# Kernel optimization log

Measured on AMD Instinct MI355X. Metric: run time of the kernel, lower is better.

## Reference

```python
import jax, jax.numpy as jnp
import numpy as np

N_NODES = 50000
N_EDGES = 800000
BATCH = 4


def setup_inputs() -> dict:
    key = jax.random.key(0)
    ks = jax.random.split(key, 12)
    inp = {
        "x": jax.random.normal(ks[0], (BATCH, N_NODES, 1, 1), dtype=jnp.float32),
        "edge_index": jax.random.randint(ks[1], (2, N_EDGES), 0, N_NODES, dtype=jnp.int64),
        "W_conv1": jax.random.normal(ks[2], (3, 1, 32), dtype=jnp.float32) * 0.1,
        "b_conv1": jnp.zeros((3, 32), dtype=jnp.float32),
        "W_lin1": jax.random.normal(ks[3], (3, 64, 32), dtype=jnp.float32) * 0.1,
        "b_lin1": jnp.zeros((3, 32), dtype=jnp.float32),
        "att1": jax.random.uniform(ks[4], (1,), dtype=jnp.float32),
        "W_conv2": jax.random.normal(ks[5], (3, 32, 32), dtype=jnp.float32) * 0.1,
        "b_conv2": jnp.zeros((3, 32), dtype=jnp.float32),
        "W_lin2": jax.random.normal(ks[6], (3, 64, 32), dtype=jnp.float32) * 0.1,
        "b_lin2": jnp.zeros((3, 32), dtype=jnp.float32),
        "att2": jax.random.uniform(ks[7], (1,), dtype=jnp.float32),
        "W_out": jax.random.normal(ks[8], (32, 1), dtype=jnp.float32) * 0.1,
        "b_out": jnp.zeros((1,), dtype=jnp.float32),
    }
    return inp


def _gcn(h, W, b, src, dst, norm, inv_deg, n):
    # h: (B,N,Fin) -> (B,N,Fout); symmetric-normalized GCNConv with self loops
    xw = h @ W                                   # (B,N,Fout)
    msg = xw[:, src, :] * norm[None, :, None]    # (B,E,Fout)
    agg = jax.ops.segment_sum(jnp.swapaxes(msg, 0, 1), dst, num_segments=n)
    agg = jnp.swapaxes(agg, 0, 1)                # (B,N,Fout)
    return agg + xw * inv_deg[None, :, None] + b


def _tgcn_cell(h_in, Wc, bc, Wl, bl, att, src, dst, norm, inv_deg, n):
    # TGCN2 GRU cell with H0 = 0, weighted by softmax(att) (periods=1 -> weight 1)
    B = h_in.shape[0]
    out_dim = Wc.shape[-1]
    H = jnp.zeros((B, n, out_dim), dtype=h_in.dtype)
    cz = _gcn(h_in, Wc[0], bc[0], src, dst, norm, inv_deg, n)
    Z = jax.nn.sigmoid(jnp.concatenate([cz, H], axis=-1) @ Wl[0] + bl[0])
    cr = _gcn(h_in, Wc[1], bc[1], src, dst, norm, inv_deg, n)
    R = jax.nn.sigmoid(jnp.concatenate([cr, H], axis=-1) @ Wl[1] + bl[1])
    ch = _gcn(h_in, Wc[2], bc[2], src, dst, norm, inv_deg, n)
    Ht = jnp.tanh(jnp.concatenate([ch, H * R], axis=-1) @ Wl[2] + bl[2])
    Hn = Z * H + (1.0 - Z) * Ht
    a = jax.nn.softmax(att)  # (1,) -> [1.0]
    return a[0] * Hn


def reference(x, edge_index, W_conv1, b_conv1, W_lin1, b_lin1, att1,
              W_conv2, b_conv2, W_lin2, b_lin2, att2, W_out, b_out):
    n = x.shape[1]
    src, dst = edge_index[0], edge_index[1]
    ones = jnp.ones(src.shape[0], dtype=x.dtype)
    deg = jax.ops.segment_sum(ones, dst, num_segments=n) + 1.0  # + self loop
    dis = jax.lax.rsqrt(deg)
    norm = dis[src] * dis[dst]   # (E,)
    inv_deg = 1.0 / deg          # self-loop norm

    h = x[..., 0]  # (B,N,1) periods=1
    h = jax.nn.relu(_tgcn_cell(h, W_conv1, b_conv1, W_lin1, b_lin1, att1,
                               src, dst, norm, inv_deg, n))
    h = jax.nn.relu(_tgcn_cell(h, W_conv2, b_conv2, W_lin2, b_lin2, att2,
                               src, dst, norm, inv_deg, n))
    return h @ W_out + b_out  # (B,N,1)
```

## Files before the change

### kernel.cpp

```cpp
#include <hip/hip_runtime.h>
#include <hip/hip_fp16.h>
#include <stdint.h>

#define N_NODES 50000
#define BATCH 4
#define CAP 64

__global__ void zero_precomp_kernel(int* __restrict__ cursor,
                                    const float* __restrict__ Wc1,
                                    const float* __restrict__ bc1,
                                    const float* __restrict__ Wl1,
                                    const float* __restrict__ bl1,
                                    const float* __restrict__ Wc2,
                                    const float* __restrict__ bc2,
                                    const float* __restrict__ Wl2,
                                    const float* __restrict__ bl2,
                                    float* __restrict__ pc, int N) {
    int i = blockIdx.x * blockDim.x + threadIdx.x;
    if (i < N) cursor[i] = 0;
    if (i >= 2240) return;
    if (i < 2048) {
        int g = i >> 10;
        int kf = i & 1023;
        int k = kf >> 5, f = kf & 31;
        int gate = g ? 2 : 0;
        float s = 0.0f;
        for (int j = 0; j < 32; ++j)
            s += Wc2[gate * 1024 + k * 32 + j] * Wl2[gate * 2048 + j * 32 + f];
        pc[i] = s;
    } else if (i < 2112) {
        int g = (i - 2048) >> 5;
        int f = i & 31;
        int gate = g ? 2 : 0;
        float s = bl2[gate * 32 + f];
        for (int j = 0; j < 32; ++j)
            s += bc2[gate * 32 + j] * Wl2[gate * 2048 + j * 32 + f];
        pc[i] = s;
    } else {
        int t = i - 2112;
        int which = t >> 5;
        int f = t & 31;
        int gate = (which >= 2) ? 2 : 0;
        if ((which & 1) == 0) {
            float s = 0.0f;
            for (int j = 0; j < 32; ++j)
                s += Wc1[gate * 32 + j] * Wl1[gate * 2048 + j * 32 + f];
            pc[i] = s;
        } else {
            float s = bl1[gate * 32 + f];
            for (int j = 0; j < 32; ++j)
                s += bc1[gate * 32 + j] * Wl1[gate * 2048 + j * 32 + f];
            pc[i] = s;
        }
    }
}

__global__ void fill_kernel(const int* __restrict__ src,
                            const int* __restrict__ dst,
                            int* __restrict__ cursor,
                            unsigned short* __restrict__ bucket, int E) {
    int e = blockIdx.x * blockDim.x + threadIdx.x;
    if (e < E) {
        int d = dst[e];
        int pos = atomicAdd(&cursor[d], 1);
        if (pos < CAP) bucket[d * CAP + pos] = (unsigned short)src[e];
    }
}

__global__ void dis_xd_kernel(const int* __restrict__ deg,
                              const float* __restrict__ x,
                              float* __restrict__ dis,
                              float4* __restrict__ xd, int N) {
    int n = blockIdx.x * blockDim.x + threadIdx.x;
    if (n >= N) return;
    float d = rsqrtf((float)(deg[n] + 1));
    dis[n] = d;
    xd[n] = make_float4(x[n] * d, x[N + n] * d, x[2 * N + n] * d,
                        x[3 * N + n] * d);
}

__global__ void s1h1_kernel(const float4* __restrict__ xd,
                            const float* __restrict__ dis,
                            const int* __restrict__ deg,
                            const unsigned short* __restrict__ bucket,
                            const float* __restrict__ pc,
                            char* __restrict__ hs, int N) {
    int idx = blockIdx.x * blockDim.x + threadIdx.x;
    int node = idx >> 3;
    if (node >= N) return;
    int j = idx & 7;
    int cnt = deg[node];
    if (cnt > CAP) cnt = CAP;
    float ax, ay, az, aw;
    if (j == 0) {
        float4 v = xd[node];
        ax = v.x; ay = v.y; az = v.z; aw = v.w;
    } else {
        ax = ay = az = aw = 0.f;
    }
    for (int i = j; i < cnt; i += 8) {
        int s = bucket[node * CAP + i];
        float4 v = xd[s];
        ax += v.x; ay += v.y; az += v.z; aw += v.w;
    }
#pragma unroll
    for (int m = 4; m; m >>= 1) {
        ax += __shfl_xor(ax, m, 64);
        ay += __shfl_xor(ay, m, 64);
        az += __shfl_xor(az, m, 64);
        aw += __shfl_xor(aw, m, 64);
    }
    float d = dis[node];
    float t0 = ax * d, t1 = ay * d, t2 = az * d, t3 = aw * d;
#pragma unroll
    for (int m = 0; m < 4; ++m) {
        int f = j + 8 * m;
        float uz = pc[2112 + f], vz = pc[2144 + f];
        float uh = pc[2176 + f], vh = pc[2208 + f];
        float h0 = fmaxf((1.0f - 1.0f / (1.0f + expf(-(t0 * uz + vz)))) *
                         tanhf(t0 * uh + vh), 0.0f) * d;
        float h1 = fmaxf((1.0f - 1.0f / (1.0f + expf(-(t1 * uz + vz)))) *
                         tanhf(t1 * uh + vh), 0.0f) * d;
        float h2 = fmaxf((1.0f - 1.0f / (1.0f + expf(-(t2 * uz + vz)))) *
                         tanhf(t2 * uh + vh), 0.0f) * d;
        float h3 = fmaxf((1.0f - 1.0f / (1.0f + expf(-(t3 * uz + vz)))) *
                         tanhf(t3 * uh + vh), 0.0f) * d;
        __half2 lo = __floats2half2_rn(h0, h1);
        __half2 hi = __floats2half2_rn(h2, h3);
        uint2 u;
        u.x = *reinterpret_cast<unsigned int*>(&lo);
        u.y = *reinterpret_cast<unsigned int*>(&hi);
        *reinterpret_cast<uint2*>(hs + (size_t)node * 256 + f * 8) = u;
    }
}

__global__ __launch_bounds__(256) void l2_agg_kernel(
    const char* __restrict__ hs, const float* __restrict__ dis,
    const int* __restrict__ deg, const unsigned short* __restrict__ bucket,
    const float* __restrict__ pc, const float* __restrict__ Wout,
    const float* __restrict__ bout, float* __restrict__ out, int N) {
    __shared__ float2 sT[4][64];
    int wv = threadIdx.x >> 6;
    int lane = threadIdx.x & 63;
    int f = lane & 31;
    int h = lane >> 5;

    float wl0[32], wl2[32];
#pragma unroll
    for (int k = 0; k < 32; ++k) {
        wl0[k] = pc[k * 32 + f];
        wl2[k] = pc[1024 + k * 32 + f];
    }
    float w0 = pc[2048 + f], w2 = pc[2080 + f];
    float wf = Wout[f];
    float bo = bout[0];
    const char* hp = hs + f * 8 + h * 4;

    int wid = (blockIdx.x * blockDim.x + threadIdx.x) >> 6;
    int nw = (gridDim.x * blockDim.x) >> 6;

    for (int node = wid; node < N; node += nw) {
        int cnt = deg[node];
        if (cnt > CAP) cnt = CAP;
        unsigned int bidx = bucket[node * CAP + lane];
        __half2 acc = *(const __half2*)(hp + (size_t)node * 256);
        int i = 0;
        for (; i + 8 <= cnt; i += 8) {
            unsigned int o0 = __builtin_amdgcn_readlane(bidx, i) * 256u;
            unsigned int o1 = __builtin_amdgcn_readlane(bidx, i + 1) * 256u;
            unsigned int o2 = __builtin_amdgcn_readlane(bidx, i + 2) * 256u;
            unsigned int o3 = __builtin_amdgcn_readlane(bidx, i + 3) * 256u;
            unsigned int o4 = __builtin_amdgcn_readlane(bidx, i + 4) * 256u;
            unsigned int o5 = __builtin_amdgcn_readlane(bidx, i + 5) * 256u;
            unsigned int o6 = __builtin_amdgcn_readlane(bidx, i + 6) * 256u;
            unsigned int o7 = __builtin_amdgcn_readlane(bidx, i + 7) * 256u;
            __half2 v0 = *(const __half2*)(hp + o0);
            __half2 v1 = *(const __half2*)(hp + o1);
            __half2 v2 = *(const __half2*)(hp + o2);
            __half2 v3 = *(const __half2*)(hp + o3);
            __half2 v4 = *(const __half2*)(hp + o4);
            __half2 v5 = *(const __half2*)(hp + o5);
            __half2 v6 = *(const __half2*)(hp + o6);
            __half2 v7 = *(const __half2*)(hp + o7);
            __half2 s01 = __hadd2(v0, v1);
            __half2 s23 = __hadd2(v2, v3);
            __half2 s45 = __hadd2(v4, v5);
            __half2 s67 = __hadd2(v6, v7);
            acc = __hadd2(acc, __hadd2(__hadd2(s01, s23), __hadd2(s45, s67)));
        }
        for (; i < cnt; ++i) {
            unsigned int o = __builtin_amdgcn_readlane(bidx, i) * 256u;
            acc = __hadd2(acc, *(const __half2*)(hp + o));
        }
        float2 fa = __half22float2(acc);

        sT[wv][lane] = fa;

        float sz0 = 0.f, sz1 = 0.f, sh0 = 0.f, sh1 = 0.f;
        const float2* tp = &sT[wv][h * 32];
#pragma unroll
        for (int k = 0; k < 32; k += 2) {
            float4 t2 = *(const float4*)&tp[k];
            sz0 += t2.x * wl0[k];     sz1 += t2.y * wl0[k];
            sh0 += t2.x * wl2[k];     sh1 += t2.y * wl2[k];
            sz0 += t2.z * wl0[k + 1]; sz1 += t2.w * wl0[k + 1];
            sh0 += t2.z * wl2[k + 1]; sh1 += t2.w * wl2[k + 1];
        }
        float dn = dis[node];
        float z0 = 1.0f / (1.0f + expf(-(dn * sz0 + w0)));
        float z1 = 1.0f / (1.0f + expf(-(dn * sz1 + w0)));
        float t0 = tanhf(dn * sh0 + w2);
        float t1 = tanhf(dn * sh1 + w2);
        float h20 = fmaxf((1.0f - z0) * t0, 0.0f);
        float h21 = fmaxf((1.0f - z1) * t1, 0.0f);

        float o0 = h20 * wf;
        float o1 = h21 * wf;
#pragma unroll
        for (int d = 16; d; d >>= 1) {
            o0 += __shfl_xor(o0, d, 64);
            o1 += __shfl_xor(o1, d, 64);
        }
        if (f == 0) {
            out[(size_t)(2 * h) * N + node] = o0 + bo;
            out[(size_t)(2 * h + 1) * N + node] = o1 + bo;
        }
    }
}


extern "C" void kernel_launch(void* const* d_in, const int* in_sizes, int n_in,
                              void* d_out, int out_size, void* d_ws,
                              size_t ws_size, hipStream_t stream) {
    const float* x    = (const float*)d_in[0];
    const int*   ei   = (const int*)d_in[1];
    const float* Wc1  = (const float*)d_in[2];
    const float* bc1  = (const float*)d_in[3];
    const float* Wl1  = (const float*)d_in[4];
    const float* bl1  = (const float*)d_in[5];
    const float* Wc2  = (const float*)d_in[7];
    const float* bc2  = (const float*)d_in[8];
    const float* Wl2  = (const float*)d_in[9];
    const float* bl2  = (const float*)d_in[10];
    const float* Wout = (const float*)d_in[12];
    const float* bout = (const float*)d_in[13];

    const int E = in_sizes[1] / 2;
    const int N = N_NODES;
    const int* src = ei;
    const int* dst = ei + E;

    char* p = (char*)d_ws;
    auto alloc = [&](size_t bytes) {
        char* r = p;
        p += (bytes + 15) & ~(size_t)15;
        return r;
    };
    int*            cursor = (int*)alloc(N * sizeof(int));
    unsigned short* bucket = (unsigned short*)alloc((size_t)N * CAP * 2);
    float*          dis    = (float*)alloc(N * sizeof(float));
    float*          xd     = (float*)alloc((size_t)N * 4 * sizeof(float));
    char*           hs     = (char*)alloc((size_t)N * 256);
    float*          pc     = (float*)alloc(2240 * sizeof(float));

    zero_precomp_kernel<<<(N + 255) / 256, 256, 0, stream>>>(
        cursor, Wc1, bc1, Wl1, bl1, Wc2, bc2, Wl2, bl2, pc, N);

    fill_kernel<<<(E + 255) / 256, 256, 0, stream>>>(src, dst, cursor, bucket,
                                                     E);
    dis_xd_kernel<<<(N + 255) / 256, 256, 0, stream>>>(cursor, x, dis,
                                                       (float4*)xd, N);
    s1h1_kernel<<<(N * 8 + 255) / 256, 256, 0, stream>>>(
        (const float4*)xd, dis, cursor, bucket, pc, hs, N);

    l2_agg_kernel<<<2048, 256, 0, stream>>>(hs, dis, cursor, bucket, pc, Wout,
                                            bout, (float*)d_out, N);
}
```

Before: 219.1 us.

## Bin neighbor lists by source chunk and process eight nodes per wave in phase

The bucket fill now splits each node's neighbor list into four sub-buckets keyed by source-node range, with a per-chunk cursor. The layer-2 aggregation has each wave handle eight nodes at once, walking the source chunks in lockstep so concurrent gathers hit a narrower slice of the feature table, which aims to improve L2/cache locality. Costs include larger cursor and bucket arrays, more atomics contention patterns, per-chunk caps of 32 that can drop edges for skewed degree, more register pressure, and a per-edge branch on counts.

New measurement: 315.1 us. 43.8% more time.

```diff
diff --git a/kernel.cpp b/kernel.cpp
--- a/kernel.cpp
+++ b/kernel.cpp
@@ -3,10 +3,14 @@
 #include <stdint.h>
 
 #define N_NODES 50000
-#define BATCH 4
-#define CAP 64
-
-__global__ void zero_precomp_kernel(int* __restrict__ cursor,
+#define NC 4
+#define CHUNK 12500
+#define SCAP 32
+#define ROWS 128
+#define ROWU 64
+#define NPW 8
+
+__global__ void zero_precomp_kernel(int* __restrict__ cursor4,
                                     const float* __restrict__ Wc1,
                                     const float* __restrict__ bc1,
                                     const float* __restrict__ Wl1,
@@ -15,9 +19,9 @@
                                     const float* __restrict__ bc2,
                                     const float* __restrict__ Wl2,
                                     const float* __restrict__ bl2,
-                                    float* __restrict__ pc, int N) {
+                                    float* __restrict__ pc, int N4) {
     int i = blockIdx.x * blockDim.x + threadIdx.x;
-    if (i < N) cursor[i] = 0;
+    if (i < N4) cursor4[i] = 0;
     if (i >= 2240) return;
     if (i < 2048) {
         int g = i >> 10;
@@ -57,23 +61,27 @@
 
 __global__ void fill_kernel(const int* __restrict__ src,
                             const int* __restrict__ dst,
-                            int* __restrict__ cursor,
+                            int* __restrict__ cursor4,
                             unsigned short* __restrict__ bucket, int E) {
     int e = blockIdx.x * blockDim.x + threadIdx.x;
     if (e < E) {
+        int s = src[e];
         int d = dst[e];
-        int pos = atomicAdd(&cursor[d], 1);
-        if (pos < CAP) bucket[d * CAP + pos] = (unsigned short)src[e];
-    }
-}
-
-__global__ void dis_xd_kernel(const int* __restrict__ deg,
+        int c = (unsigned)s / (unsigned)CHUNK;
+        int pos = atomicAdd(&cursor4[d * 4 + c], 1);
+        if (pos < SCAP) bucket[(size_t)d * ROWS + c * SCAP + pos] = (unsigned short)s;
+    }
+}
+
+__global__ void dis_xd_kernel(const int4* __restrict__ cursor4,
                               const float* __restrict__ x,
                               float* __restrict__ dis,
                               float4* __restrict__ xd, int N) {
     int n = blockIdx.x * blockDim.x + threadIdx.x;
     if (n >= N) return;
-    float d = rsqrtf((float)(deg[n] + 1));
+    int4 cc = cursor4[n];
+    int deg = cc.x + cc.y + cc.z + cc.w;
+    float d = rsqrtf((float)(deg + 1));
     dis[n] = d;
     xd[n] = make_float4(x[n] * d, x[N + n] * d, x[2 * N + n] * d,
                         x[3 * N + n] * d);
@@ -81,7 +89,7 @@
 
 __global__ void s1h1_kernel(const float4* __restrict__ xd,
                             const float* __restrict__ dis,
-                            const int* __restrict__ deg,
+                            const int4* __restrict__ cursor4,
                             const unsigned short* __restrict__ bucket,
                             const float* __restrict__ pc,
                             char* __restrict__ hs, int N) {
@@ -89,8 +97,9 @@
     int node = idx >> 3;
     if (node >= N) return;
     int j = idx & 7;
-    int cnt = deg[node];
-    if (cnt > CAP) cnt = CAP;
+    int4 cc = cursor4[node];
+    int cn[4] = {min(cc.x, SCAP), min(cc.y, SCAP), min(cc.z, SCAP),
+                 min(cc.w, SCAP)};
     float ax, ay, az, aw;
     if (j == 0) {
         float4 v = xd[node];
@@ -98,10 +107,14 @@
     } else {
         ax = ay = az = aw = 0.f;
     }
-    for (int i = j; i < cnt; i += 8) {
-        int s = bucket[node * CAP + i];
-        float4 v = xd[s];
-        ax += v.x; ay += v.y; az += v.z; aw += v.w;
+#pragma unroll
+    for (int c = 0; c < NC; ++c) {
+        int cnt = cn[c];
+        for (int i = j; i < cnt; i += 8) {
+            int s = bucket[(size_t)node * ROWS + c * SCAP + i];
+            float4 v = xd[s];
+            ax += v.x; ay += v.y; az += v.z; aw += v.w;
+        }
     }
 #pragma unroll
     for (int m = 4; m; m >>= 1) {
@@ -136,7 +149,7 @@
 
 __global__ __launch_bounds__(256) void l2_agg_kernel(
     const char* __restrict__ hs, const float* __restrict__ dis,
-    const int* __restrict__ deg, const unsigned short* __restrict__ bucket,
+    const int4* __restrict__ cursor4, const uint32_t* __restrict__ bucket,
     const float* __restrict__ pc, const float* __restrict__ Wout,
     const float* __restrict__ bout, float* __restrict__ out, int N) {
     __shared__ float2 sT[4][64];
@@ -157,75 +170,98 @@
     const char* hp = hs + f * 8 + h * 4;
 
     int wid = (blockIdx.x * blockDim.x + threadIdx.x) >> 6;
-    int nw = (gridDim.x * blockDim.x) >> 6;
-
-    for (int node = wid; node < N; node += nw) {
-        int cnt = deg[node];
-        if (cnt > CAP) cnt = CAP;
-        unsigned int bidx = bucket[node * CAP + lane];
-        __half2 acc = *(const __half2*)(hp + (size_t)node * 256);
-        int i = 0;
-        for (; i + 8 <= cnt; i += 8) {
-            unsigned int o0 = __builtin_amdgcn_readlane(bidx, i) * 256u;
-            unsigned int o1 = __builtin_amdgcn_readlane(bidx, i + 1) * 256u;
-            unsigned int o2 = __builtin_amdgcn_readlane(bidx, i + 2) * 256u;
-            unsigned int o3 = __builtin_amdgcn_readlane(bidx, i + 3) * 256u;
-            unsigned int o4 = __builtin_amdgcn_readlane(bidx, i + 4) * 256u;
-            unsigned int o5 = __builtin_amdgcn_readlane(bidx, i + 5) * 256u;
-            unsigned int o6 = __builtin_amdgcn_readlane(bidx, i + 6) * 256u;
-            unsigned int o7 = __builtin_amdgcn_readlane(bidx, i + 7) * 256u;
-            __half2 v0 = *(const __half2*)(hp + o0);
-            __half2 v1 = *(const __half2*)(hp + o1);
-            __half2 v2 = *(const __half2*)(hp + o2);
-            __half2 v3 = *(const __half2*)(hp + o3);
-            __half2 v4 = *(const __half2*)(hp + o4);
-            __half2 v5 = *(const __half2*)(hp + o5);
-            __half2 v6 = *(const __half2*)(hp + o6);
-            __half2 v7 = *(const __half2*)(hp + o7);
-            __half2 s01 = __hadd2(v0, v1);
-            __half2 s23 = __hadd2(v2, v3);
-            __half2 s45 = __hadd2(v4, v5);
-            __half2 s67 = __hadd2(v6, v7);
-            acc = __hadd2(acc, __hadd2(__hadd2(s01, s23), __hadd2(s45, s67)));
+    int n0 = wid * NPW;
+    if (n0 >= N) return;
+
+#define DECL(J)                                                              \
+    __half2 acc##J = __floats2half2_rn(0.f, 0.f);                            \
+    uint32_t bx##J = 0, cp##J = 0;                                           \
+    int cs##J = 0;                                                           \
+    {                                                                        \
+        int n = n0 + J;                                                      \
+        if (n < N) {                                                         \
+            int4 cc = cursor4[n];                                            \
+            int a0 = min(cc.x, SCAP), a1 = min(cc.y, SCAP);                  \
+            int a2 = min(cc.z, SCAP), a3 = min(cc.w, SCAP);                  \
+            cp##J = (uint32_t)(a0 | (a1 << 8) | (a2 << 16) | (a3 << 24));    \
+            bx##J = bucket[(size_t)n * ROWU + lane];                         \
+            cs##J = (int)((unsigned)n / (unsigned)CHUNK);                    \
+        }                                                                    \
+    }
+    DECL(0) DECL(1) DECL(2) DECL(3) DECL(4) DECL(5) DECL(6) DECL(7)
+#undef DECL
+
+    for (int c = 0; c < NC; ++c) {
+        int lb = c * 16;
+#define SELF(J)                                                              \
+    {                                                                        \
+        int n = n0 + J;                                                      \
+        if (n < N && cs##J == c)                                             \
+            acc##J = __hadd2(acc##J,                                         \
+                             *(const __half2*)(hp + (size_t)n * 256));       \
+    }
+        SELF(0) SELF(1) SELF(2) SELF(3) SELF(4) SELF(5) SELF(6) SELF(7)
+#undef SELF
+        int c0_ = (int)((cp0 >> (8 * c)) & 255u);
+        int c1_ = (int)((cp1 >> (8 * c)) & 255u);
+        int c2_ = (int)((cp2 >> (8 * c)) & 255u);
+        int c3_ = (int)((cp3 >> (8 * c)) & 255u);
+        int c4_ = (int)((cp4 >> (8 * c)) & 255u);
+        int c5_ = (int)((cp5 >> (8 * c)) & 255u);
+        int c6_ = (int)((cp6 >> (8 * c)) & 255u);
+        int c7_ = (int)((cp7 >> (8 * c)) & 255u);
+        int mc = max(max(max(c0_, c1_), max(c2_, c3_)),
+                     max(max(c4_, c5_), max(c6_, c7_)));
+        for (int s_ = 0; s_ < mc; ++s_) {
+            int w_ = lb + (s_ >> 1);
+            int hi = s_ & 1;
+#define EDGE(J)                                                              \
+    if (s_ < c##J##_) {                                                      \
+        uint32_t ww = __builtin_amdgcn_readlane(bx##J, w_);                  \
+        uint32_t ix = hi ? (ww >> 16) : (ww & 0xffffu);                      \
+        acc##J = __hadd2(acc##J, *(const __half2*)(hp + ix * 256u));         \
+    }
+            EDGE(0) EDGE(1) EDGE(2) EDGE(3) EDGE(4) EDGE(5) EDGE(6) EDGE(7)
+#undef EDGE
         }
-        for (; i < cnt; ++i) {
-            unsigned int o = __builtin_amdgcn_readlane(bidx, i) * 256u;
-            acc = __hadd2(acc, *(const __half2*)(hp + o));
-        }
-        float2 fa = __half22float2(acc);
-
-        sT[wv][lane] = fa;
-
-        float sz0 = 0.f, sz1 = 0.f, sh0 = 0.f, sh1 = 0.f;
-        const float2* tp = &sT[wv][h * 32];
-#pragma unroll
-        for (int k = 0; k < 32; k += 2) {
-            float4 t2 = *(const float4*)&tp[k];
-            sz0 += t2.x * wl0[k];     sz1 += t2.y * wl0[k];
-            sh0 += t2.x * wl2[k];     sh1 += t2.y * wl2[k];
-            sz0 += t2.z * wl0[k + 1]; sz1 += t2.w * wl0[k + 1];
-            sh0 += t2.z * wl2[k + 1]; sh1 += t2.w * wl2[k + 1];
-        }
-        float dn = dis[node];
-        float z0 = 1.0f / (1.0f + expf(-(dn * sz0 + w0)));
-        float z1 = 1.0f / (1.0f + expf(-(dn * sz1 + w0)));
-        float t0 = tanhf(dn * sh0 + w2);
-        float t1 = tanhf(dn * sh1 + w2);
-        float h20 = fmaxf((1.0f - z0) * t0, 0.0f);
-        float h21 = fmaxf((1.0f - z1) * t1, 0.0f);
-
-        float o0 = h20 * wf;
-        float o1 = h21 * wf;
-#pragma unroll
-        for (int d = 16; d; d >>= 1) {
-            o0 += __shfl_xor(o0, d, 64);
-            o1 += __shfl_xor(o1, d, 64);
-        }
-        if (f == 0) {
-            out[(size_t)(2 * h) * N + node] = o0 + bo;
-            out[(size_t)(2 * h + 1) * N + node] = o1 + bo;
-        }
-    }
+    }
+
+#define TAIL(J)                                                              \
+    {                                                                        \
+        int n = n0 + J;                                                      \
+        if (n < N) {                                                         \
+            float2 fa = __half22float2(acc##J);                              \
+            sT[wv][lane] = fa;                                               \
+            float sz0 = 0.f, sz1 = 0.f, sh0 = 0.f, sh1 = 0.f;                \
+            const float2* tp = &sT[wv][h * 32];                              \
+            _Pragma("unroll") for (int k = 0; k < 32; k += 2) {              \
+                float4 t2 = *(const float4*)&tp[k];                          \
+                sz0 += t2.x * wl0[k];     sz1 += t2.y * wl0[k];              \
+                sh0 += t2.x * wl2[k];     sh1 += t2.y * wl2[k];              \
+                sz0 += t2.z * wl0[k + 1]; sz1 += t2.w * wl0[k + 1];          \
+                sh0 += t2.z * wl2[k + 1]; sh1 += t2.w * wl2[k + 1];          \
+            }                                                                \
+            float dn = dis[n];                                               \
+            float z0 = 1.0f / (1.0f + expf(-(dn * sz0 + w0)));               \
+            float z1 = 1.0f / (1.0f + expf(-(dn * sz1 + w0)));               \
+            float t0 = tanhf(dn * sh0 + w2);                                 \
+            float t1 = tanhf(dn * sh1 + w2);                                 \
+            float h20 = fmaxf((1.0f - z0) * t0, 0.0f);                       \
+            float h21 = fmaxf((1.0f - z1) * t1, 0.0f);                       \
+            float o0 = h20 * wf;                                             \
+            float o1 = h21 * wf;                                             \
+            _Pragma("unroll") for (int d_ = 16; d_; d_ >>= 1) {              \
+                o0 += __shfl_xor(o0, d_, 64);                                \
+                o1 += __shfl_xor(o1, d_, 64);                                \
+            }                                                                \
+            if (f == 0) {                                                    \
+                out[(size_t)(2 * h) * N + n] = o0 + bo;                      \
+                out[(size_t)(2 * h + 1) * N + n] = o1 + bo;                  \
+            }                                                                \
+        }                                                                    \
+    }
+    TAIL(0) TAIL(1) TAIL(2) TAIL(3) TAIL(4) TAIL(5) TAIL(6) TAIL(7)
+#undef TAIL
 }
 
 
@@ -256,23 +292,25 @@
         p += (bytes + 15) & ~(size_t)15;
         return r;
     };
-    int*            cursor = (int*)alloc(N * sizeof(int));
-    unsigned short* bucket = (unsigned short*)alloc((size_t)N * CAP * 2);
-    float*          dis    = (float*)alloc(N * sizeof(float));
-    float*          xd     = (float*)alloc((size_t)N * 4 * sizeof(float));
-    char*           hs     = (char*)alloc((size_t)N * 256);
-    float*          pc     = (float*)alloc(2240 * sizeof(float));
-
-    zero_precomp_kernel<<<(N + 255) / 256, 256, 0, stream>>>(
-        cursor, Wc1, bc1, Wl1, bl1, Wc2, bc2, Wl2, bl2, pc, N);
-
-    fill_kernel<<<(E + 255) / 256, 256, 0, stream>>>(src, dst, cursor, bucket,
+    int*            cursor4 = (int*)alloc((size_t)N * 4 * sizeof(int));
+    unsigned short* bucket  = (unsigned short*)alloc((size_t)N * ROWS * 2);
+    float*          dis     = (float*)alloc(N * sizeof(float));
+    float*          xd      = (float*)alloc((size_t)N * 4 * sizeof(float));
+    char*           hs      = (char*)alloc((size_t)N * 256);
+    float*          pc      = (float*)alloc(2240 * sizeof(float));
+
+    zero_precomp_kernel<<<(4 * N + 255) / 256, 256, 0, stream>>>(
+        cursor4, Wc1, bc1, Wl1, bl1, Wc2, bc2, Wl2, bl2, pc, 4 * N);
+
+    fill_kernel<<<(E + 255) / 256, 256, 0, stream>>>(src, dst, cursor4, bucket,
                                                      E);
-    dis_xd_kernel<<<(N + 255) / 256, 256, 0, stream>>>(cursor, x, dis,
-                                                       (float4*)xd, N);
+    dis_xd_kernel<<<(N + 255) / 256, 256, 0, stream>>>((const int4*)cursor4, x,
+                                                       dis, (float4*)xd, N);
     s1h1_kernel<<<(N * 8 + 255) / 256, 256, 0, stream>>>(
-        (const float4*)xd, dis, cursor, bucket, pc, hs, N);
-
-    l2_agg_kernel<<<2048, 256, 0, stream>>>(hs, dis, cursor, bucket, pc, Wout,
-                                            bout, (float*)d_out, N);
-}
+        (const float4*)xd, dis, (const int4*)cursor4, bucket, pc, hs, N);
+
+    int blocks = (N + NPW * 4 - 1) / (NPW * 4);
+    l2_agg_kernel<<<blocks, 256, 0, stream>>>(
+        hs, dis, (const int4*)cursor4, (const uint32_t*)bucket, pc, Wout, bout,
+        (float*)d_out, N);
+}
```
